# Kernel tuning notes

Measured on AMD Instinct MI355X. Metric: run time of the kernel, lower is better.

Reference implementation:

```python
import jax, jax.numpy as jnp
import numpy as np

TEMPERATURE = 0.05
BETA = 1.0
LAMBDA_THRESHOLD = 0.7
EPS = 1e-8


def setup_inputs() -> dict:
    key = jax.random.key(0)
    k1, k2 = jax.random.split(key)
    B, D = 8192, 256
    features = jax.random.normal(k1, (B, D), dtype=jnp.float32)
    labels = jax.random.randint(k2, (B,), 0, 100, dtype=jnp.int64)
    return {"features": features, "labels": labels}


def reference(features, labels):
    B = features.shape[0]
    # L2-normalize rows
    f = features / jnp.linalg.norm(features, axis=1, keepdims=True)
    sim = jnp.matmul(f, f.T) / TEMPERATURE                      # [B, B]
    pos_mask = (labels[:, None] == labels[None, :]).astype(f.dtype)
    eye = jnp.eye(B, dtype=f.dtype)
    pos_mask = pos_mask - eye                                    # positives, no diagonal
    exp_sim = jnp.exp(sim) * (1.0 - eye)                         # diag zeroed
    denom = jnp.sum(exp_sim, axis=1, keepdims=True)              # [B, 1]
    # SCL term: -sum over positive pairs of log(exp_sim[i,j] / (denom_i + eps))
    # log(exp_sim/(denom+eps)) = sim - log(denom+eps) for off-diagonal entries
    per_pair = jnp.log(denom + EPS) - sim                        # [B, B]
    num_pos = jnp.sum(pos_mask)
    scl_loss = jnp.sum(pos_mask * per_pair)
    scl_loss = jnp.where(num_pos > 0, scl_loss / num_pos, 0.0)
    # Relaxation term: rows with too-similar positives
    high_sim = ((sim * TEMPERATURE) > LAMBDA_THRESHOLD) & (pos_mask > 0)
    high_f = high_sim.astype(f.dtype)
    row_sum = jnp.sum(exp_sim * high_f, axis=1)                  # [B]
    self_term = jnp.exp(jnp.asarray(1.0 / TEMPERATURE, dtype=f.dtype))
    row_log = jnp.where(row_sum > 0, jnp.log(row_sum + self_term), 0.0)
    n_high = jnp.sum(high_f)
    relax_loss = jnp.where(n_high > 0, jnp.sum(row_log) / n_high, 0.0)
    total = scl_loss + BETA * relax_loss
    return total
```

## Files before the change

### kernel.cpp

```cpp
#include <hip/hip_runtime.h>
#include <hip/hip_bf16.h>
#include <math.h>

typedef short bf16x8 __attribute__((ext_vector_type(8)));
typedef float f32x16 __attribute__((ext_vector_type(16)));

#define NB 8192
#define ND 256
#define NCLSR 100
#define BK 64
#define ES 136
#define INV_T 20.0f
#define LOG2E_T 28.853900817779268f
#define HI_THR 1.2026042e6f
#define SELF_TERM 4.85165195e8f


__global__ __launch_bounds__(256) void normalize_kernel(
    const float* __restrict__ feat, unsigned short* __restrict__ fb,
    float* __restrict__ hsum, float* __restrict__ nhighf,
    float* __restrict__ scal) {
    const int wave = threadIdx.x >> 6;
    const int lane = threadIdx.x & 63;
    const int row  = blockIdx.x * 4 + wave;
    float4 v = reinterpret_cast<const float4*>(feat + (size_t)row * ND)[lane];
    float ss = v.x * v.x + v.y * v.y + v.z * v.z + v.w * v.w;
    #pragma unroll
    for (int off = 32; off > 0; off >>= 1) ss += __shfl_xor(ss, off);
    const float inv = rsqrtf(ss);
    ushort4 o;
    __hip_bfloat16 h0 = __float2bfloat16(v.x * inv); o.x = *reinterpret_cast<unsigned short*>(&h0);
    __hip_bfloat16 h1 = __float2bfloat16(v.y * inv); o.y = *reinterpret_cast<unsigned short*>(&h1);
    __hip_bfloat16 h2 = __float2bfloat16(v.z * inv); o.z = *reinterpret_cast<unsigned short*>(&h2);
    __hip_bfloat16 h3 = __float2bfloat16(v.w * inv); o.w = *reinterpret_cast<unsigned short*>(&h3);
    reinterpret_cast<ushort4*>(fb + (size_t)row * ND)[lane] = o;
    if (blockIdx.x < 32) {
        const int i = (blockIdx.x << 8) + threadIdx.x;
        hsum[i] = 0.f;
        nhighf[i] = 0.f;
    } else if (blockIdx.x == 32 && threadIdx.x < 6) {
        scal[threadIdx.x] = 0.f;
    }
}

__global__ __launch_bounds__(256, 2) void sim_kernel(
    const unsigned short* __restrict__ fb, const int* __restrict__ labels,
    float* __restrict__ Q, float* __restrict__ hsum,
    float* __restrict__ nhighf, float* __restrict__ scal) {
    __shared__ __align__(16) unsigned short ldsU[128 * ES];
    __shared__ float ldsCol[2][128];
    __shared__ float ldsRowF[128];
    __shared__ int   ldsLab[256];
    __shared__ float ldsP[4];
    unsigned short* ldsA = ldsU;
    unsigned short* ldsB = ldsU + 128 * BK;
    unsigned short* ldsE = ldsU;

    const int t = blockIdx.x;
    int bi = (int)((sqrtf((float)(8 * t + 1)) - 1.0f) * 0.5f);
    while ((bi + 1) * (bi + 2) / 2 <= t) ++bi;
    while (bi * (bi + 1) / 2 > t) --bi;
    const int bj = t - bi * (bi + 1) / 2;
    const int I0 = bi << 7;
    const int J0 = bj << 7;
    const bool isdiag = (bi == bj);

    const int tid  = threadIdx.x;
    const int wave = tid >> 6;
    const int lane = tid & 63;
    const int wy = wave >> 1;
    const int wx = wave & 1;
    const int l31  = lane & 31;
    const int half = lane >> 5;

    if (tid < 128) ldsLab[tid] = labels[I0 + tid];
    else           ldsLab[tid] = labels[J0 + tid - 128];

    int offRC[4];
    #pragma unroll
    for (int c = 0; c < 4; ++c) {
        const int Lg = (c << 6) + lane;
        const int row_loc = (wave << 5) + (Lg >> 3);
        const int g = (Lg & 7) ^ ((Lg >> 3) & 7);
        offRC[c] = row_loc * ND + (g << 3);
    }
    const unsigned short* baseA = fb + (size_t)I0 * ND;
    const unsigned short* baseB = fb + (size_t)J0 * ND;

    f32x16 acc[2][2];
    #pragma unroll
    for (int fy = 0; fy < 2; ++fy)
        #pragma unroll
        for (int fx = 0; fx < 2; ++fx)
            #pragma unroll
            for (int e = 0; e < 16; ++e) acc[fy][fx][e] = 0.f;

    for (int kk = 0; kk < ND; kk += BK) {
        __syncthreads();
        #pragma unroll
        for (int c = 0; c < 4; ++c) {
            __builtin_amdgcn_global_load_lds(
                (const __attribute__((address_space(1))) void*)(baseA + offRC[c] + kk),
                (__attribute__((address_space(3))) void*)(ldsA + (wave << 11) + (c << 9)),
                16, 0, 0);
            __builtin_amdgcn_global_load_lds(
                (const __attribute__((address_space(1))) void*)(baseB + offRC[c] + kk),
                (__attribute__((address_space(3))) void*)(ldsB + (wave << 11) + (c << 9)),
                16, 0, 0);
        }
        __syncthreads();

        #pragma unroll
        for (int s = 0; s < 4; ++s) {
            const int gp = ((s << 1) + half) ^ (l31 & 7);
            bf16x8 a[2], b[2];
            #pragma unroll
            for (int f = 0; f < 2; ++f) {
                const int rowA = (wy << 6) + (f << 5) + l31;
                const int rowB = (wx << 6) + (f << 5) + l31;
                a[f] = *reinterpret_cast<const bf16x8*>(ldsA + rowA * BK + (gp << 3));
                b[f] = *reinterpret_cast<const bf16x8*>(ldsB + rowB * BK + (gp << 3));
            }
            #pragma unroll
            for (int fy = 0; fy < 2; ++fy)
                #pragma unroll
                for (int fx = 0; fx < 2; ++fx)
                    acc[fy][fx] = __builtin_amdgcn_mfma_f32_32x32x16_bf16(
                        a[fy], b[fx], acc[fy][fx], 0, 0, 0);
        }
    }
    __syncthreads();

    int ccol[2], lcol[2];
    #pragma unroll
    for (int fx = 0; fx < 2; ++fx) {
        ccol[fx] = (wx << 6) + (fx << 5) + l31;
        lcol[fx] = ldsLab[128 + ccol[fx]];
    }
    unsigned short* ePtr0 = ldsE + (half << 2) * ES + ccol[0];
    unsigned short* ePtr1 = ldsE + (half << 2) * ES + ccol[1];

    float cs[2] = {0.f, 0.f};
    float pp = 0.f;

    if (!isdiag) {
        #pragma unroll
        for (int fy = 0; fy < 2; ++fy) {
            const int rbase = (wy << 6) + (fy << 5) + (half << 2);
            int4 lr[4];
            #pragma unroll
            for (int g = 0; g < 4; ++g)
                lr[g] = *reinterpret_cast<const int4*>(&ldsLab[rbase + (g << 3)]);
            #pragma unroll
            for (int reg = 0; reg < 16; ++reg) {
                const int g = reg >> 2, idx = reg & 3;
                const int lrow = (idx == 0) ? lr[g].x : (idx == 1) ? lr[g].y
                               : (idx == 2) ? lr[g].z : lr[g].w;
                const int roff = (wy << 6) + (fy << 5) + idx + (g << 3);
                #pragma unroll
                for (int fx = 0; fx < 2; ++fx) {
                    const float a = acc[fy][fx][reg];
                    const float e = exp2f(a * LOG2E_T);
                    cs[fx] += e;
                    if (lcol[fx] == lrow) pp += a;
                    __hip_bfloat16 h = __float2bfloat16(e);
                    (fx ? ePtr1 : ePtr0)[roff * ES] = *reinterpret_cast<unsigned short*>(&h);
                }
            }
        }
    } else {
        #pragma unroll
        for (int fy = 0; fy < 2; ++fy) {
            #pragma unroll
            for (int reg = 0; reg < 16; ++reg) {
                const int rloc = (reg & 3) + ((reg >> 2) << 3) + (half << 2);
                const int row_local = (wy << 6) + (fy << 5) + rloc;
                const int lrow = ldsLab[row_local];
                #pragma unroll
                for (int fx = 0; fx < 2; ++fx) {
                    const bool dband = (((wy << 1) + fy) == ((wx << 1) + fx));
                    const bool diag_el = dband && (l31 == rloc);
                    const float a = acc[fy][fx][reg];
                    float e = exp2f(a * LOG2E_T);
                    if (diag_el) e = 0.f;
                    cs[fx] += e;
                    if (lcol[fx] == lrow && !diag_el) pp += a;
                    __hip_bfloat16 h = __float2bfloat16(e);
                    ldsE[row_local * ES + ccol[fx]] = *reinterpret_cast<unsigned short*>(&h);
                }
            }
        }
    }
    const int anyhigh = (cs[0] > HI_THR) || (cs[1] > HI_THR);
    #pragma unroll
    for (int fx = 0; fx < 2; ++fx) cs[fx] += __shfl_xor(cs[fx], 32);
    if (half == 0) {
        ldsCol[wy][ccol[0]] = cs[0];
        ldsCol[wy][ccol[1]] = cs[1];
    }
    #pragma unroll
    for (int off = 32; off > 0; off >>= 1) pp += __shfl_xor(pp, off);
    if (lane == 0) ldsP[wave] = pp;

    if (__any(anyhigh)) {
        #pragma unroll
        for (int fy = 0; fy < 2; ++fy) {
            #pragma unroll
            for (int reg = 0; reg < 16; ++reg) {
                const int rloc = (reg & 3) + ((reg >> 2) << 3) + (half << 2);
                const int row_local = (wy << 6) + (fy << 5) + rloc;
                const int lrow = ldsLab[row_local];
                #pragma unroll
                for (int fx = 0; fx < 2; ++fx) {
                    const bool dband = isdiag && (((wy << 1) + fy) == ((wx << 1) + fx));
                    const bool diag_el = dband && (l31 == rloc);
                    const float a = acc[fy][fx][reg];
                    if (a > 0.7f && lcol[fx] == lrow && !diag_el) {
                        const float e2 = exp2f(a * LOG2E_T);
                        atomicAdd(&hsum[I0 + row_local], e2);
                        atomicAdd(&nhighf[I0 + row_local], 1.f);
                        if (!isdiag) {
                            atomicAdd(&hsum[J0 + ccol[fx]], e2);
                            atomicAdd(&nhighf[J0 + ccol[fx]], 1.f);
                        }
                    }
                }
            }
        }
    }
    __syncthreads();

    {
        bf16x8 ones;
        #pragma unroll
        for (int j = 0; j < 8; ++j) ones[j] = (short)0x3F80;
        f32x16 rs;
        #pragma unroll
        for (int e = 0; e < 16; ++e) rs[e] = 0.f;
        const int rE = (wave << 5) + l31;
        const unsigned short* rPtr = ldsE + rE * ES + (half << 3);
        #pragma unroll
        for (int kc = 0; kc < 8; ++kc) {
            bf16x8 bE = *reinterpret_cast<const bf16x8*>(rPtr + (kc << 4));
            rs = __builtin_amdgcn_mfma_f32_32x32x16_bf16(ones, bE, rs, 0, 0, 0);
        }
        if (half == 0) ldsRowF[rE] = rs[0];
    }
    __syncthreads();

    if (tid < 128) {
        Q[(size_t)(bi * 64 + bj) * 128 + tid] = ldsRowF[tid];
    } else if (!isdiag) {
        const int c2 = tid - 128;
        Q[(size_t)(bj * 64 + bi) * 128 + c2] = ldsCol[0][c2] + ldsCol[1][c2];
    }
    if (tid == 0) {
        const float scale = isdiag ? 1.f : 2.f;
        atomicAdd(&scal[0], (ldsP[0] + ldsP[1] + ldsP[2] + ldsP[3]) * scale);
    }
}

__global__ __launch_bounds__(256) void finalize_kernel(
    const float* __restrict__ Q, const float* __restrict__ hsum,
    const float* __restrict__ nhighf, const int* __restrict__ labels,
    float* __restrict__ scal, float* __restrict__ out) {
    const int g = blockIdx.x;
    const int tid = threadIdx.x;
    __shared__ int cnt[128];
    if (tid < 128) cnt[tid] = 0;
    __syncthreads();
    for (int i = tid; i < NB; i += 256)
        atomicAdd(&cnt[labels[i]], 1);
    const int r = tid & 127;
    const int sh = tid >> 7;
    const float* base = Q + (size_t)g * 64 * 128;
    float s = 0.f;
    #pragma unroll 8
    for (int i = 0; i < 32; ++i)
        s += base[(size_t)(sh * 32 + i) * 128 + r];
    __shared__ float red[256];
    red[tid] = s;
    __syncthreads();
    float SL = 0.f, RL = 0.f, NH = 0.f, NT = 0.f;
    if (tid < 128) {
        const float denom = red[tid] + red[tid + 128];
        const int i = (g << 7) + tid;
        const float np = (float)(cnt[labels[i]] - 1);
        SL = np * logf(denom + 1e-8f);
        const float h = hsum[i];
        if (h > 0.f) RL = logf(h + SELF_TERM);
        NH = nhighf[i];
    }
    if (g == 0 && tid < NCLSR) {
        const float nc = (float)cnt[tid];
        NT = nc * (nc - 1.f);
    }
    #pragma unroll
    for (int off = 32; off > 0; off >>= 1) {
        SL += __shfl_xor(SL, off); RL += __shfl_xor(RL, off);
        NH += __shfl_xor(NH, off); NT += __shfl_xor(NT, off);
    }
    __shared__ float part[4][4];
    if ((tid & 63) == 0) {
        int w = tid >> 6;
        part[w][0] = SL; part[w][1] = RL; part[w][2] = NH; part[w][3] = NT;
    }
    __syncthreads();
    if (tid == 0) {
        float sl = part[0][0] + part[1][0] + part[2][0] + part[3][0];
        float rl = part[0][1] + part[1][1] + part[2][1] + part[3][1];
        float nh = part[0][2] + part[1][2] + part[2][2] + part[3][2];
        float nt = part[0][3] + part[1][3] + part[2][3] + part[3][3];
        atomicAdd(&scal[1], sl);
        atomicAdd(&scal[2], rl);
        atomicAdd(&scal[3], nh);
        if (g == 0) atomicAdd(&scal[4], nt);
        __threadfence();
        const int ticket = atomicAdd((int*)(scal + 5), 1);
        if (ticket == 63) {
            const float SLt = atomicAdd(&scal[1], 0.f);
            const float RLt = atomicAdd(&scal[2], 0.f);
            const float NHt = atomicAdd(&scal[3], 0.f);
            const float NTt = atomicAdd(&scal[4], 0.f);
            const float pos = atomicAdd(&scal[0], 0.f) * INV_T;
            const float scl   = (NTt > 0.f) ? (SLt - pos) / NTt : 0.f;
            const float relax = (NHt > 0.f) ? RLt / NHt : 0.f;
            out[0] = scl + relax;
        }
    }
}

extern "C" void kernel_launch(void* const* d_in, const int* in_sizes, int n_in,
                              void* d_out, int out_size, void* d_ws, size_t ws_size,
                              hipStream_t stream) {
    const float* feat  = (const float*)d_in[0];
    const int* labels  = (const int*)d_in[1];
    float* out = (float*)d_out;

    char* ws = (char*)d_ws;
    unsigned short* fb = (unsigned short*)ws;
    float* Q      = (float*)(ws + (size_t)NB * ND * sizeof(unsigned short));
    float* hsum   = Q + 64 * 64 * 128;
    float* nhighf = hsum + NB;
    float* scal   = nhighf + NB;

    normalize_kernel<<<NB / 4, 256, 0, stream>>>(feat, fb, hsum, nhighf, scal);
    sim_kernel<<<2080, 256, 0, stream>>>(fb, labels, Q, hsum, nhighf, scal);
    finalize_kernel<<<64, 256, 0, stream>>>(Q, hsum, nhighf, labels, scal, out);
}
```

Baseline: 117.1 us.

## Compute transposed tile via extra MFMAs to get row sums without LDS staging

Instead of writing bf16 exp values to LDS and reducing rows with a ones-vector MFMA pass, the kernel computes a second transposed accumulator (B·Aᵀ) alongside the main one. Row sums then come from per-lane reductions, like the column sums. This removes the LDS write/read of the exp tile, an extra barrier, and the bf16 rounding of exp values. In exchange it doubles the MFMA count in the main loop, doubles accumulator registers (64 more VGPRs, which could hurt occupancy at 2 blocks per CU), and doubles the exp2 evaluations.

```diff
diff --git a/kernel.cpp b/kernel.cpp
--- a/kernel.cpp
+++ b/kernel.cpp
@@ -9,7 +9,6 @@
 #define ND 256
 #define NCLSR 100
 #define BK 64
-#define ES 136
 #define INV_T 20.0f
 #define LOG2E_T 28.853900817779268f
 #define HI_THR 1.2026042e6f
@@ -47,14 +46,12 @@
     const unsigned short* __restrict__ fb, const int* __restrict__ labels,
     float* __restrict__ Q, float* __restrict__ hsum,
     float* __restrict__ nhighf, float* __restrict__ scal) {
-    __shared__ __align__(16) unsigned short ldsU[128 * ES];
+    __shared__ __align__(16) unsigned short ldsA[128 * BK];
+    __shared__ __align__(16) unsigned short ldsB[128 * BK];
+    __shared__ float ldsRow[2][128];
     __shared__ float ldsCol[2][128];
-    __shared__ float ldsRowF[128];
     __shared__ int   ldsLab[256];
     __shared__ float ldsP[4];
-    unsigned short* ldsA = ldsU;
-    unsigned short* ldsB = ldsU + 128 * BK;
-    unsigned short* ldsE = ldsU;
 
     const int t = blockIdx.x;
     int bi = (int)((sqrtf((float)(8 * t + 1)) - 1.0f) * 0.5f);
@@ -88,12 +85,13 @@
     const unsigned short* baseB = fb + (size_t)J0 * ND;
 
     f32x16 acc[2][2];
+    f32x16 accT[2][2];
     #pragma unroll
     for (int fy = 0; fy < 2; ++fy)
         #pragma unroll
         for (int fx = 0; fx < 2; ++fx)
             #pragma unroll
-            for (int e = 0; e < 16; ++e) acc[fy][fx][e] = 0.f;
+            for (int e = 0; e < 16; ++e) { acc[fy][fx][e] = 0.f; accT[fx][fy][e] = 0.f; }
 
     for (int kk = 0; kk < ND; kk += BK) {
         __syncthreads();
@@ -124,12 +122,14 @@
             #pragma unroll
             for (int fy = 0; fy < 2; ++fy)
                 #pragma unroll
-                for (int fx = 0; fx < 2; ++fx)
-                    acc[fy][fx] = __builtin_amdgcn_mfma_f32_32x32x16_bf16(
+                for (int fx = 0; fx < 2; ++fx) {
+                    acc[fy][fx]  = __builtin_amdgcn_mfma_f32_32x32x16_bf16(
                         a[fy], b[fx], acc[fy][fx], 0, 0, 0);
-        }
-    }
-    __syncthreads();
+                    accT[fx][fy] = __builtin_amdgcn_mfma_f32_32x32x16_bf16(
+                        b[fx], a[fy], accT[fx][fy], 0, 0, 0);
+                }
+        }
+    }
 
     int ccol[2], lcol[2];
     #pragma unroll
@@ -137,10 +137,9 @@
         ccol[fx] = (wx << 6) + (fx << 5) + l31;
         lcol[fx] = ldsLab[128 + ccol[fx]];
     }
-    unsigned short* ePtr0 = ldsE + (half << 2) * ES + ccol[0];
-    unsigned short* ePtr1 = ldsE + (half << 2) * ES + ccol[1];
 
     float cs[2] = {0.f, 0.f};
+    float rs[2] = {0.f, 0.f};
     float pp = 0.f;
 
     if (!isdiag) {
@@ -156,15 +155,12 @@
                 const int g = reg >> 2, idx = reg & 3;
                 const int lrow = (idx == 0) ? lr[g].x : (idx == 1) ? lr[g].y
                                : (idx == 2) ? lr[g].z : lr[g].w;
-                const int roff = (wy << 6) + (fy << 5) + idx + (g << 3);
                 #pragma unroll
                 for (int fx = 0; fx < 2; ++fx) {
-                    const float a = acc[fy][fx][reg];
-                    const float e = exp2f(a * LOG2E_T);
-                    cs[fx] += e;
-                    if (lcol[fx] == lrow) pp += a;
-                    __hip_bfloat16 h = __float2bfloat16(e);
-                    (fx ? ePtr1 : ePtr0)[roff * ES] = *reinterpret_cast<unsigned short*>(&h);
+                    const float av = acc[fy][fx][reg];
+                    cs[fx] += exp2f(av * LOG2E_T);
+                    if (lcol[fx] == lrow) pp += av;
+                    rs[fy] += exp2f(accT[fx][fy][reg] * LOG2E_T);
                 }
             }
         }
@@ -180,23 +176,29 @@
                 for (int fx = 0; fx < 2; ++fx) {
                     const bool dband = (((wy << 1) + fy) == ((wx << 1) + fx));
                     const bool diag_el = dband && (l31 == rloc);
-                    const float a = acc[fy][fx][reg];
-                    float e = exp2f(a * LOG2E_T);
+                    const float av = acc[fy][fx][reg];
+                    float e = exp2f(av * LOG2E_T);
                     if (diag_el) e = 0.f;
                     cs[fx] += e;
-                    if (lcol[fx] == lrow && !diag_el) pp += a;
-                    __hip_bfloat16 h = __float2bfloat16(e);
-                    ldsE[row_local * ES + ccol[fx]] = *reinterpret_cast<unsigned short*>(&h);
+                    if (lcol[fx] == lrow && !diag_el) pp += av;
+                    float eT = exp2f(accT[fx][fy][reg] * LOG2E_T);
+                    if (diag_el) eT = 0.f;
+                    rs[fy] += eT;
                 }
             }
         }
     }
     const int anyhigh = (cs[0] > HI_THR) || (cs[1] > HI_THR);
     #pragma unroll
-    for (int fx = 0; fx < 2; ++fx) cs[fx] += __shfl_xor(cs[fx], 32);
+    for (int f = 0; f < 2; ++f) {
+        cs[f] += __shfl_xor(cs[f], 32);
+        rs[f] += __shfl_xor(rs[f], 32);
+    }
     if (half == 0) {
         ldsCol[wy][ccol[0]] = cs[0];
         ldsCol[wy][ccol[1]] = cs[1];
+        ldsRow[wx][(wy << 6) + l31]      = rs[0];
+        ldsRow[wx][(wy << 6) + 32 + l31] = rs[1];
     }
     #pragma unroll
     for (int off = 32; off > 0; off >>= 1) pp += __shfl_xor(pp, off);
@@ -214,9 +216,9 @@
                 for (int fx = 0; fx < 2; ++fx) {
                     const bool dband = isdiag && (((wy << 1) + fy) == ((wx << 1) + fx));
                     const bool diag_el = dband && (l31 == rloc);
-                    const float a = acc[fy][fx][reg];
-                    if (a > 0.7f && lcol[fx] == lrow && !diag_el) {
-                        const float e2 = exp2f(a * LOG2E_T);
+                    const float av = acc[fy][fx][reg];
+                    if (av > 0.7f && lcol[fx] == lrow && !diag_el) {
+                        const float e2 = exp2f(av * LOG2E_T);
                         atomicAdd(&hsum[I0 + row_local], e2);
                         atomicAdd(&nhighf[I0 + row_local], 1.f);
                         if (!isdiag) {
@@ -230,26 +232,8 @@
     }
     __syncthreads();
 
-    {
-        bf16x8 ones;
-        #pragma unroll
-        for (int j = 0; j < 8; ++j) ones[j] = (short)0x3F80;
-        f32x16 rs;
-        #pragma unroll
-        for (int e = 0; e < 16; ++e) rs[e] = 0.f;
-        const int rE = (wave << 5) + l31;
-        const unsigned short* rPtr = ldsE + rE * ES + (half << 3);
-        #pragma unroll
-        for (int kc = 0; kc < 8; ++kc) {
-            bf16x8 bE = *reinterpret_cast<const bf16x8*>(rPtr + (kc << 4));
-            rs = __builtin_amdgcn_mfma_f32_32x32x16_bf16(ones, bE, rs, 0, 0, 0);
-        }
-        if (half == 0) ldsRowF[rE] = rs[0];
-    }
-    __syncthreads();
-
     if (tid < 128) {
-        Q[(size_t)(bi * 64 + bj) * 128 + tid] = ldsRowF[tid];
+        Q[(size_t)(bi * 64 + bj) * 128 + tid] = ldsRow[0][tid] + ldsRow[1][tid];
     } else if (!isdiag) {
         const int c2 = tid - 128;
         Q[(size_t)(bj * 64 + bi) * 128 + c2] = ldsCol[0][c2] + ldsCol[1][c2];
```

New measurement: 125.9 us. +7.6%, slower.
